# Kernel tuning notes

Hardware: AMD Instinct MI355X
Metric: run time of the kernel (lower is better)

Reference implementation:

```python
import jax, jax.numpy as jnp
import numpy as np

KMIX = 16
N_CH = 302   # hardcoded number of output channels in MDNLayer
N_POS = 394  # hardcoded evaluation grid size


def setup_inputs() -> dict:
    key = jax.random.key(0)
    k1, k2 = jax.random.split(key)
    B, D = 32, 1024
    units = N_CH * KMIX * 3  # 14496
    x = jax.random.normal(k1, (B, D), dtype=jnp.float32)
    # 'random_normal' keras initializer uses stddev=0.05
    w = jax.random.normal(k2, (D, units), dtype=jnp.float32) * 0.05
    b = jnp.zeros((units,), dtype=jnp.float32)
    return {"x": x, "w": w, "b": b}


def reference(x, w, b):
    B = x.shape[0]
    # Dense projection then reshape to (B, 3*KMIX, 302) as in the original
    y = (x @ w + b).reshape(B, 3 * KMIX, N_CH)
    mu = y[:, 0 * KMIX:1 * KMIX, :]   # (B, K, 302)
    sig = y[:, 1 * KMIX:2 * KMIX, :]  # (B, K, 302) used raw as Normal scale
    pi = y[:, 2 * KMIX:3 * KMIX, :]   # (B, K, 302) mixture logits

    pos = jnp.linspace(0.0, 1.0, N_POS, dtype=x.dtype)  # (394,)
    inv_sqrt_2pi = jnp.asarray(1.0 / np.sqrt(2.0 * np.pi), dtype=x.dtype)

    # Per-component Normal pdf at each grid point: (B, K, 302, 394)
    z = (pos[None, None, None, :] - mu[..., None]) / sig[..., None]
    comp_pdf = jnp.exp(-0.5 * z * z) * (inv_sqrt_2pi / sig[..., None])

    # Mixture weights: softmax over the K components (axis=1)
    weights = jax.nn.softmax(pi, axis=1)  # (B, K, 302)

    # Weighted sum over components -> (B, 302, 394)
    res = jnp.einsum('bkc,bkcp->bcp', weights, comp_pdf)
    return res[..., None]  # (B, 302, 394, 1)
```

## Files before the change

kernel.cpp:

```cpp
#include <hip/hip_runtime.h>

#define BATCH 32
#define DIM 1024
#define NCH 302
#define KMIX 16
#define UNITS (NCH * KMIX * 3)
#define NPOS 394
#define NTILE 32
#define NSLICE 16
#define DSLICE (DIM / NSLICE)

#if __has_builtin(__builtin_amdgcn_exp2f)
__device__ __forceinline__ float fast_exp_neghalf_sq(float t) {
  return __builtin_amdgcn_exp2f(t * t * (-0.72134752044448170f));
}
#else
__device__ __forceinline__ float fast_exp_neghalf_sq(float t) {
  return __expf(-0.5f * t * t);
}
#endif

__global__ __launch_bounds__(512) void gemm_kernel(
    const float* __restrict__ x, const float* __restrict__ w,
    const float* __restrict__ bias, float* __restrict__ y)
{
  __shared__ float red[NSLICE][BATCH][NTILE];
  const int tid   = threadIdx.x;
  const int col   = tid & 31;
  const int slice = tid >> 5;
  const int n0    = blockIdx.x * NTILE;
  const int dbase = slice * DSLICE;

  float acc[BATCH];
#pragma unroll
  for (int b = 0; b < BATCH; ++b) acc[b] = 0.0f;

  const float* wp = w + (size_t)dbase * UNITS + n0 + col;
  const float* xp = x + dbase;

  float wv[8], wn[8];
#pragma unroll
  for (int j = 0; j < 8; ++j) wv[j] = wp[(size_t)j * UNITS];

  for (int dd0 = 0; dd0 < DSLICE; dd0 += 8) {
    const int nxt = dd0 + 8;
    if (nxt < DSLICE) {
#pragma unroll
      for (int j = 0; j < 8; ++j) wn[j] = wp[(size_t)(nxt + j) * UNITS];
    }
#pragma unroll
    for (int b = 0; b < BATCH; ++b) {
      const float* xr = xp + b * DIM + dd0;
      const float4 x0 = *(const float4*)(xr);
      const float4 x1 = *(const float4*)(xr + 4);
      acc[b] = fmaf(x0.x, wv[0], acc[b]);
      acc[b] = fmaf(x0.y, wv[1], acc[b]);
      acc[b] = fmaf(x0.z, wv[2], acc[b]);
      acc[b] = fmaf(x0.w, wv[3], acc[b]);
      acc[b] = fmaf(x1.x, wv[4], acc[b]);
      acc[b] = fmaf(x1.y, wv[5], acc[b]);
      acc[b] = fmaf(x1.z, wv[6], acc[b]);
      acc[b] = fmaf(x1.w, wv[7], acc[b]);
    }
#pragma unroll
    for (int j = 0; j < 8; ++j) wv[j] = wn[j];
  }

#pragma unroll
  for (int b = 0; b < BATCH; ++b) red[slice][b][col] = acc[b];
  __syncthreads();

#pragma unroll
  for (int i = 0; i < 2; ++i) {
    const int oi = tid + i * 512;
    const int b  = oi >> 5;
    const int c  = oi & 31;
    float s = 0.0f;
#pragma unroll
    for (int sl = 0; sl < NSLICE; ++sl) s += red[sl][b][c];
    y[b * UNITS + n0 + c] = s + bias[n0 + c];
  }
}

__global__ __launch_bounds__(256) void mdn_kernel(
    const float* __restrict__ y, float* __restrict__ out)
{
  const int lane = threadIdx.x & 63;
  int pair = blockIdx.x * 4 + (threadIdx.x >> 6);
  pair = __builtin_amdgcn_readfirstlane(pair);
  const int b = pair / NCH;
  const int c = pair - b * NCH;
  const float* yb = y + b * UNITS + c;

  float pi[KMIX];
  float m = -3.4e38f;
#pragma unroll
  for (int k = 0; k < KMIX; ++k) {
    pi[k] = yb[(2 * KMIX + k) * NCH];
    m = fmaxf(m, pi[k]);
  }
  float s = 0.0f;
#pragma unroll
  for (int k = 0; k < KMIX; ++k) { pi[k] = __expf(pi[k] - m); s += pi[k]; }
  const float inv_s = 1.0f / s;

  const float inv_sqrt_2pi = 0.39894228040143267f;
  float A[KMIX], B2[KMIX], C[KMIX];
#pragma unroll
  for (int k = 0; k < KMIX; ++k) {
    const float mu   = yb[k * NCH];
    const float sig  = yb[(KMIX + k) * NCH];
    const float isig = 1.0f / sig;
    A[k]  = isig;
    B2[k] = -mu * isig;
    C[k]  = pi[k] * inv_s * inv_sqrt_2pi * isig;
  }

  float* op = out + (size_t)pair * NPOS;
  for (int p = lane; p < NPOS; p += 64) {
    const float pos = (float)p * (1.0f / (NPOS - 1));
    float acc = 0.0f;
#pragma unroll
    for (int k = 0; k < KMIX; ++k) {
      const float t = fmaf(pos, A[k], B2[k]);
      acc = fmaf(C[k], fast_exp_neghalf_sq(t), acc);
    }
    op[p] = acc;
  }
}

extern "C" void kernel_launch(void* const* d_in, const int* in_sizes, int n_in,
                              void* d_out, int out_size, void* d_ws, size_t ws_size,
                              hipStream_t stream) {
  const float* x    = (const float*)d_in[0];
  const float* w    = (const float*)d_in[1];
  const float* bias = (const float*)d_in[2];
  float* out = (float*)d_out;
  float* y   = (float*)d_ws;

  gemm_kernel<<<UNITS / NTILE, 512, 0, stream>>>(x, w, bias, y);
  mdn_kernel<<<(BATCH * NCH) / 4, 256, 0, stream>>>(y, out);
}
```

Before: 173.4 us.

## Restructure GEMM as split-K with LDS-staged x, float4 tiles and separate reduction

The GEMM is rewritten to use 2D grid split-K: each block stages a 32x128 slice of x in LDS, and each thread computes a 4-column by 8-batch register tile, loading w as float4. Partial sums are written to the output buffer as scratch, then a new reduce kernel sums the 8 partials and adds bias. The MDN kernel is also restructured so the component loop is outer and all 7 position slots are accumulated in registers. This raises memory-level parallelism and register reuse on the weight stream, at the cost of an extra launch and extra partial-sum traffic.

New measurement: 152.3 us. -12.2%, faster.

```diff
diff --git a/kernel.cpp b/kernel.cpp
--- a/kernel.cpp
+++ b/kernel.cpp
@@ -4,82 +4,102 @@
 #define DIM 1024
 #define NCH 302
 #define KMIX 16
-#define UNITS (NCH * KMIX * 3)
+#define UNITS 14496
 #define NPOS 394
-#define NTILE 32
-#define NSLICE 16
-#define DSLICE (DIM / NSLICE)
+#define KSPLIT 8
+#define KCHUNK (DIM / KSPLIT)
+#define NTILE 256
+#define NTILES ((UNITS + NTILE - 1) / NTILE)
+#define BSUB 8
 
-#if __has_builtin(__builtin_amdgcn_exp2f)
-__device__ __forceinline__ float fast_exp_neghalf_sq(float t) {
-  return __builtin_amdgcn_exp2f(t * t * (-0.72134752044448170f));
-}
-#else
-__device__ __forceinline__ float fast_exp_neghalf_sq(float t) {
-  return __expf(-0.5f * t * t);
-}
-#endif
+__global__ __launch_bounds__(256) void gemm_kernel(
+    const float* __restrict__ x, const float* __restrict__ w,
+    float* __restrict__ partial)
+{
+  __shared__ float xs[BATCH][KCHUNK];
+  const int tid = threadIdx.x;
+  const int k0  = blockIdx.y * KCHUNK;
+  const int n0  = blockIdx.x * NTILE;
 
-__global__ __launch_bounds__(512) void gemm_kernel(
-    const float* __restrict__ x, const float* __restrict__ w,
-    const float* __restrict__ bias, float* __restrict__ y)
-{
-  __shared__ float red[NSLICE][BATCH][NTILE];
-  const int tid   = threadIdx.x;
-  const int col   = tid & 31;
-  const int slice = tid >> 5;
-  const int n0    = blockIdx.x * NTILE;
-  const int dbase = slice * DSLICE;
+#pragma unroll
+  for (int j = 0; j < 4; ++j) {
+    const int idx4 = tid + j * 256;
+    const int b    = idx4 >> 5;
+    const int d4   = idx4 & 31;
+    const float4 v = *(const float4*)(x + b * DIM + k0 + d4 * 4);
+    *(float4*)(&xs[b][d4 * 4]) = v;
+  }
+  __syncthreads();
 
-  float acc[BATCH];
+  const int lane = tid & 63;
+  const int bg   = tid >> 6;
+  const bool st  = (n0 + lane * 4) < UNITS;
+  int nc = n0 + lane * 4;
+  if (nc > UNITS - 4) nc = UNITS - 4;
+
+  float4 acc[BSUB];
 #pragma unroll
-  for (int b = 0; b < BATCH; ++b) acc[b] = 0.0f;
+  for (int bi = 0; bi < BSUB; ++bi) acc[bi] = make_float4(0.f, 0.f, 0.f, 0.f);
 
-  const float* wp = w + (size_t)dbase * UNITS + n0 + col;
-  const float* xp = x + dbase;
+  const float* wp = w + (size_t)k0 * UNITS + nc;
+  float4 wv[4], wn[4];
+#pragma unroll
+  for (int j = 0; j < 4; ++j) wv[j] = *(const float4*)(wp + (size_t)j * UNITS);
 
-  float wv[8], wn[8];
+  for (int dd = 0; dd < KCHUNK; dd += 4) {
+    if (dd + 4 < KCHUNK) {
 #pragma unroll
-  for (int j = 0; j < 8; ++j) wv[j] = wp[(size_t)j * UNITS];
-
-  for (int dd0 = 0; dd0 < DSLICE; dd0 += 8) {
-    const int nxt = dd0 + 8;
-    if (nxt < DSLICE) {
-#pragma unroll
-      for (int j = 0; j < 8; ++j) wn[j] = wp[(size_t)(nxt + j) * UNITS];
+      for (int j = 0; j < 4; ++j)
+        wn[j] = *(const float4*)(wp + (size_t)(dd + 4 + j) * UNITS);
     }
 #pragma unroll
-    for (int b = 0; b < BATCH; ++b) {
-      const float* xr = xp + b * DIM + dd0;
-      const float4 x0 = *(const float4*)(xr);
-      const float4 x1 = *(const float4*)(xr + 4);
-      acc[b] = fmaf(x0.x, wv[0], acc[b]);
-      acc[b] = fmaf(x0.y, wv[1], acc[b]);
-      acc[b] = fmaf(x0.z, wv[2], acc[b]);
-      acc[b] = fmaf(x0.w, wv[3], acc[b]);
-      acc[b] = fmaf(x1.x, wv[4], acc[b]);
-      acc[b] = fmaf(x1.y, wv[5], acc[b]);
-      acc[b] = fmaf(x1.z, wv[6], acc[b]);
-      acc[b] = fmaf(x1.w, wv[7], acc[b]);
+    for (int bi = 0; bi < BSUB; ++bi) {
+      const float4 xv = *(const float4*)(&xs[bg * BSUB + bi][dd]);
+      acc[bi].x = fmaf(xv.x, wv[0].x, acc[bi].x);
+      acc[bi].y = fmaf(xv.x, wv[0].y, acc[bi].y);
+      acc[bi].z = fmaf(xv.x, wv[0].z, acc[bi].z);
+      acc[bi].w = fmaf(xv.x, wv[0].w, acc[bi].w);
+      acc[bi].x = fmaf(xv.y, wv[1].x, acc[bi].x);
+      acc[bi].y = fmaf(xv.y, wv[1].y, acc[bi].y);
+      acc[bi].z = fmaf(xv.y, wv[1].z, acc[bi].z);
+      acc[bi].w = fmaf(xv.y, wv[1].w, acc[bi].w);
+      acc[bi].x = fmaf(xv.z, wv[2].x, acc[bi].x);
+      acc[bi].y = fmaf(xv.z, wv[2].y, acc[bi].y);
+      acc[bi].z = fmaf(xv.z, wv[2].z, acc[bi].z);
+      acc[bi].w = fmaf(xv.z, wv[2].w, acc[bi].w);
+      acc[bi].x = fmaf(xv.w, wv[3].x, acc[bi].x);
+      acc[bi].y = fmaf(xv.w, wv[3].y, acc[bi].y);
+      acc[bi].z = fmaf(xv.w, wv[3].z, acc[bi].z);
+      acc[bi].w = fmaf(xv.w, wv[3].w, acc[bi].w);
     }
 #pragma unroll
-    for (int j = 0; j < 8; ++j) wv[j] = wn[j];
+    for (int j = 0; j < 4; ++j) wv[j] = wn[j];
   }
 
+  if (st) {
+    float* pp = partial + ((size_t)blockIdx.y * BATCH + bg * BSUB) * UNITS + nc;
 #pragma unroll
-  for (int b = 0; b < BATCH; ++b) red[slice][b][col] = acc[b];
-  __syncthreads();
+    for (int bi = 0; bi < BSUB; ++bi)
+      *(float4*)(pp + (size_t)bi * UNITS) = acc[bi];
+  }
+}
 
+__global__ __launch_bounds__(256) void reduce_kernel(
+    const float* __restrict__ partial, const float* __restrict__ bias,
+    float* __restrict__ y)
+{
+  const int f4   = blockIdx.x * 256 + threadIdx.x;
+  const int base = f4 * 4;
+  float4 s = make_float4(0.f, 0.f, 0.f, 0.f);
 #pragma unroll
-  for (int i = 0; i < 2; ++i) {
-    const int oi = tid + i * 512;
-    const int b  = oi >> 5;
-    const int c  = oi & 31;
-    float s = 0.0f;
-#pragma unroll
-    for (int sl = 0; sl < NSLICE; ++sl) s += red[sl][b][c];
-    y[b * UNITS + n0 + c] = s + bias[n0 + c];
+  for (int k = 0; k < KSPLIT; ++k) {
+    const float4 v = *(const float4*)(partial + (size_t)k * (BATCH * UNITS) + base);
+    s.x += v.x; s.y += v.y; s.z += v.z; s.w += v.w;
   }
+  const int n = base % UNITS;
+  const float4 bv = *(const float4*)(bias + n);
+  s.x += bv.x; s.y += bv.y; s.z += bv.z; s.w += bv.w;
+  *(float4*)(y + base) = s;
 }
 
 __global__ __launch_bounds__(256) void mdn_kernel(
@@ -92,40 +112,43 @@
   const int c = pair - b * NCH;
   const float* yb = y + b * UNITS + c;
 
-  float pi[KMIX];
+  float pw[KMIX];
   float m = -3.4e38f;
 #pragma unroll
   for (int k = 0; k < KMIX; ++k) {
-    pi[k] = yb[(2 * KMIX + k) * NCH];
-    m = fmaxf(m, pi[k]);
+    pw[k] = yb[(2 * KMIX + k) * NCH];
+    m = fmaxf(m, pw[k]);
   }
-  float s = 0.0f;
+  float ssum = 0.0f;
 #pragma unroll
-  for (int k = 0; k < KMIX; ++k) { pi[k] = __expf(pi[k] - m); s += pi[k]; }
-  const float inv_s = 1.0f / s;
+  for (int k = 0; k < KMIX; ++k) { pw[k] = __expf(pw[k] - m); ssum += pw[k]; }
+  const float wnorm = 0.39894228040143267f / ssum;
 
-  const float inv_sqrt_2pi = 0.39894228040143267f;
-  float A[KMIX], B2[KMIX], C[KMIX];
+  float posv[7];
+#pragma unroll
+  for (int i = 0; i < 7; ++i)
+    posv[i] = (float)(lane + i * 64) * (1.0f / (NPOS - 1));
+
+  float acc[7] = {0.f, 0.f, 0.f, 0.f, 0.f, 0.f, 0.f};
 #pragma unroll
   for (int k = 0; k < KMIX; ++k) {
     const float mu   = yb[k * NCH];
     const float sig  = yb[(KMIX + k) * NCH];
     const float isig = 1.0f / sig;
-    A[k]  = isig;
-    B2[k] = -mu * isig;
-    C[k]  = pi[k] * inv_s * inv_sqrt_2pi * isig;
+    const float coef = pw[k] * wnorm * isig;
+    const float nmu  = -mu * isig;
+#pragma unroll
+    for (int i = 0; i < 7; ++i) {
+      const float t = fmaf(posv[i], isig, nmu);
+      acc[i] = fmaf(coef, exp2f(t * t * -0.72134752044448170f), acc[i]);
+    }
   }
 
   float* op = out + (size_t)pair * NPOS;
-  for (int p = lane; p < NPOS; p += 64) {
-    const float pos = (float)p * (1.0f / (NPOS - 1));
-    float acc = 0.0f;
 #pragma unroll
-    for (int k = 0; k < KMIX; ++k) {
-      const float t = fmaf(pos, A[k], B2[k]);
-      acc = fmaf(C[k], fast_exp_neghalf_sq(t), acc);
-    }
-    op[p] = acc;
+  for (int i = 0; i < 7; ++i) {
+    const int p = lane + i * 64;
+    if (p < NPOS) op[p] = acc[i];
   }
 }
 
@@ -135,9 +158,11 @@
   const float* x    = (const float*)d_in[0];
   const float* w    = (const float*)d_in[1];
   const float* bias = (const float*)d_in[2];
-  float* out = (float*)d_out;
-  float* y   = (float*)d_ws;
+  float* out     = (float*)d_out;
+  float* partial = (float*)d_out;
+  float* y       = (float*)d_ws;
 
-  gemm_kernel<<<UNITS / NTILE, 512, 0, stream>>>(x, w, bias, y);
+  gemm_kernel<<<dim3(NTILES, KSPLIT), 256, 0, stream>>>(x, w, partial);
+  reduce_kernel<<<(BATCH * UNITS / 4) / 256, 256, 0, stream>>>(partial, bias, y);
   mdn_kernel<<<(BATCH * NCH) / 4, 256, 0, stream>>>(y, out);
 }
```
